# Kernel optimization log

Hardware: AMD Instinct MI355X
Metric: run time of the kernel (lower is better)

The kernel has to match this reference:

```python
import jax, jax.numpy as jnp
import numpy as np

NOTE_RES = 64  # global constant in the original repo; equals D of rep


def _down(x):
    # conv1d with kernel [0.5, 0.5], stride 2 over last axis (even length)
    return 0.5 * (x[..., ::2] + x[..., 1::2])


def setup_inputs() -> dict:
    key = jax.random.key(0)
    k1, k2, k3 = jax.random.split(key, 3)
    B, D, T = 32, NOTE_RES, 4096
    rep = jax.random.normal(k1, (B, D, T), dtype=jnp.float32)
    duration_mask = jax.random.uniform(k2, (B, D, T), dtype=jnp.float32)
    position_mask = jax.random.uniform(k3, (B, D, T), dtype=jnp.float32)
    return {
        "rep": rep,
        "duration_mask": duration_mask,
        "position_mask": position_mask,
        "low_duration": 1,
        "up_duration": 64,
    }


def reference(rep, duration_mask, position_mask, low_duration, up_duration):
    B, D, T = rep.shape  # D == NOTE_RES
    x = jnp.transpose(rep, (0, 2, 1))  # [B, T, NOTE_RES]; conv axis is last
    densed = _down(x)                  # [B, T, NOTE_RES//2]
    pot = NOTE_RES // 2
    res = jnp.zeros((B, T), dtype=rep.dtype)
    for i in range(0, NOTE_RES - low_duration):
        win_len = NOTE_RES - i - 1
        if win_len == pot:
            # descend one pyramid level
            x = densed
            densed = _down(x) if i < NOTE_RES - 2 else None
            d = x  # [B, T, win_len]
            pot //= 2
        else:
            pad_len = win_len - pot
            # mix fine-resolution prefix with coarse suffix -> length win_len
            d = jnp.concatenate([x[..., : 2 * pad_len], densed[..., pad_len:]], axis=-1)
        if win_len < up_duration:
            # sum_w d[b,t,w] * position_mask[b,w,t], gated by duration_mask[b,win_len-1,t]
            contrib = duration_mask[:, win_len - 1, :] * jnp.einsum(
                "btw,bwt->bt", d, position_mask[:, :win_len, :]
            )
            res = res + contrib
    return res[:, None, :]  # [B, 1, T]
```

## Files before the change

kernel.cpp:

```cpp
#include <hip/hip_runtime.h>


#define TT 4096

template <int K0>
__device__ __forceinline__ float roleK(const float* __restrict__ lrep,
                                       const float* __restrict__ lpm,
                                       const float* __restrict__ ldm, int lane,
                                       int low, int up) {
  constexpr int PADN = (K0 + 8 < 32) ? (K0 + 8) : 32;
  constexpr int PMN = (2 * K0 + 14 < 62 ? 2 * K0 + 14 : 62) - K0 + 1;
  float xa[8];
#pragma unroll
  for (int i = 0; i < 8; ++i)
    xa[i] = 0.5f * (lrep[(2 * (K0 + i)) * 64 + lane] +
                    lrep[(2 * (K0 + i) + 1) * 64 + lane]);
  float pmv[PMN];
#pragma unroll
  for (int r = 0; r < PMN; ++r) pmv[r] = lpm[(K0 + r) * 64 + lane];
  float res = 0.f;
#pragma unroll
  for (int pad = 0; pad < PADN; ++pad) {
    const int L = 32 + pad;
    const int kk0 = (pad > K0) ? pad : K0;
    float s = 0.f;
#pragma unroll
    for (int k = kk0; k < K0 + 8; ++k)
      s = fmaf(xa[k - K0], pmv[k + pad - K0], s);
    if (L >= low && L < up) res = fmaf(ldm[(31 + pad) * 64 + lane], s, res);
  }
  return res;
}

__device__ __forceinline__ float role3(const float* __restrict__ lrep,
                                       const float* __restrict__ lpm,
                                       const float* __restrict__ ldm, int lane,
                                       int low, int up) {
  float pmv[31];
#pragma unroll
  for (int r = 0; r < 31; ++r) pmv[r] = lpm[r * 64 + lane];
  float x1[32];
#pragma unroll
  for (int j = 0; j < 32; ++j)
    x1[j] = 0.5f * (lrep[(2 * j) * 64 + lane] + lrep[(2 * j + 1) * 64 + lane]);
  float res = 0.f;
#pragma unroll
  for (int pad = 0; pad < 8; ++pad) {
    const int L = 32 + pad;
    float s = 0.f;
#pragma unroll
    for (int k = pad; k < 8; ++k) s = fmaf(x1[k], pmv[k + pad], s);
    if (L >= low && L < up) res = fmaf(ldm[(31 + pad) * 64 + lane], s, res);
  }
  float x2[16], q1[16];
#pragma unroll
  for (int j = 0; j < 16; ++j) {
    const float a = x1[2 * j], bb = x1[2 * j + 1];
    x2[j] = 0.5f * (a + bb);
    q1[j] = a * pmv[2 * j] + bb * pmv[2 * j + 1];
  }
  float p = 0.f;
#pragma unroll
  for (int pad = 0; pad < 16; ++pad) {
    const int L = 16 + pad;
    float s = p;
#pragma unroll
    for (int k = pad; k < 16; ++k) s = fmaf(x2[k], pmv[k + pad], s);
    if (L >= low && L < up) res = fmaf(ldm[(15 + pad) * 64 + lane], s, res);
    p += q1[pad];
  }
  return res;
}

__device__ __forceinline__ float role4(const float* __restrict__ lrep,
                                       const float* __restrict__ lpm,
                                       const float* __restrict__ ldm, int lane,
                                       int low, int up) {
  float res = 0.f, p = 0.f;
#pragma unroll
  for (int pad = 1; pad < 32; ++pad) {
    const int j = pad - 1;
    p = fmaf(lrep[(2 * j) * 64 + lane], lpm[(2 * j) * 64 + lane],
             fmaf(lrep[(2 * j + 1) * 64 + lane], lpm[(2 * j + 1) * 64 + lane],
                  p));
    const int L = 32 + pad;
    if (L >= low && L < up) res = fmaf(ldm[(31 + pad) * 64 + lane], p, res);
  }
  return res;
}

template <int M>
__device__ __forceinline__ void level_step(const float* pmv,
                                           const float* __restrict__ ldm,
                                           int lane, int low, int up, float* xf,
                                           float* xc, float& res) {
  float q[M];
#pragma unroll
  for (int j = 0; j < M; ++j) {
    const float a = xf[2 * j], bb = xf[2 * j + 1];
    xc[j] = 0.5f * (a + bb);
    q[j] = a * pmv[2 * j] + bb * pmv[2 * j + 1];
  }
  float p = 0.f;
#pragma unroll
  for (int pad = 0; pad < M; ++pad) {
    const int L = M + pad;
    float s = p;
#pragma unroll
    for (int k = pad; k < M; ++k) s = fmaf(xc[k], pmv[k + pad], s);
    if (L >= low && L < up) res = fmaf(ldm[(M - 1 + pad) * 64 + lane], s, res);
    p += q[pad];
  }
}

__device__ __forceinline__ float role5(const float* __restrict__ lrep,
                                       const float* __restrict__ lpm,
                                       const float* __restrict__ ldm, int lane,
                                       int low, int up) {
  float pmv[15];
#pragma unroll
  for (int r = 0; r < 15; ++r) pmv[r] = lpm[r * 64 + lane];
  float x1[32];
#pragma unroll
  for (int j = 0; j < 32; ++j)
    x1[j] = 0.5f * (lrep[(2 * j) * 64 + lane] + lrep[(2 * j + 1) * 64 + lane]);
  float x2[16];
#pragma unroll
  for (int j = 0; j < 16; ++j) x2[j] = 0.5f * (x1[2 * j] + x1[2 * j + 1]);
  float res = 0.f;
  float x3[8], x4[4], x5[2], x6[1];
  level_step<8>(pmv, ldm, lane, low, up, x2, x3, res);
  level_step<4>(pmv, ldm, lane, low, up, x3, x4, res);
  level_step<2>(pmv, ldm, lane, low, up, x4, x5, res);
  level_step<1>(pmv, ldm, lane, low, up, x5, x6, res);
  return res;
}

__global__ __launch_bounds__(384, 3) void ContextGenerator_34875134444049_kernel(
    const float* __restrict__ rep, const float* __restrict__ dm,
    const float* __restrict__ pm, const int* __restrict__ lowp,
    const int* __restrict__ upp, float* __restrict__ out) {
  __shared__ float lds[192 * 64 + 6 * 64];
  const int tid = threadIdx.x;
  const int wid = tid >> 6;
  const int lane = tid & 63;
  const int b = blockIdx.x >> 6;
  const int t0 = (blockIdx.x & 63) << 6;
  const size_t base = (size_t)b * 64 * TT + (size_t)t0;

  float4 v[8];
#pragma unroll
  for (int g = 0; g < 8; ++g) {
    const int slot = tid + 384 * g;
    const int row = slot >> 4;
    const int c4 = (slot & 15) << 2;
    const float* tb = (row < 64) ? rep + base + (size_t)row * TT
                    : (row < 128) ? pm + base + (size_t)(row - 64) * TT
                                  : dm + base + (size_t)(row - 128) * TT;
    v[g] = *(const float4*)(tb + c4);
  }
#pragma unroll
  for (int g = 0; g < 8; ++g) {
    const int slot = tid + 384 * g;
    *(float4*)(&lds[slot << 2]) = v[g];
  }

  const int low = lowp[0];
  const int up = upp[0];

  __syncthreads();

  const float* lrep = lds;
  const float* lpm = lds + 64 * 64;
  const float* ldm = lds + 128 * 64;
  float* part = lds + 192 * 64;

  float res;
  if (wid == 0)
    res = roleK<24>(lrep, lpm, ldm, lane, low, up);
  else if (wid == 1)
    res = roleK<16>(lrep, lpm, ldm, lane, low, up);
  else if (wid == 2)
    res = roleK<8>(lrep, lpm, ldm, lane, low, up);
  else if (wid == 3)
    res = role3(lrep, lpm, ldm, lane, low, up);
  else if (wid == 4)
    res = role4(lrep, lpm, ldm, lane, low, up);
  else
    res = role5(lrep, lpm, ldm, lane, low, up);

  if (wid > 0) part[wid * 64 + lane] = res;
  __syncthreads();
  if (wid == 0)
    out[(size_t)b * TT + t0 + lane] = res + part[64 + lane] + part[128 + lane] +
                                      part[192 + lane] + part[256 + lane] +
                                      part[320 + lane];
}

extern "C" void kernel_launch(void* const* d_in, const int* in_sizes, int n_in,
                              void* d_out, int out_size, void* d_ws,
                              size_t ws_size, hipStream_t stream) {
  const float* rep = (const float*)d_in[0];
  const float* dm = (const float*)d_in[1];
  const float* pm = (const float*)d_in[2];
  const int* lowp = (const int*)d_in[3];
  const int* upp = (const int*)d_in[4];
  float* out = (float*)d_out;

  const int blocks = out_size / 64;
  ContextGenerator_34875134444049_kernel<<<blocks, 384, 0, stream>>>(
      rep, dm, pm, lowp, upp, out);
}
```

Before: 122.6 us.

## Make blocks persistent over four chunks and prefetch the next chunk during compute

Each block now handles four consecutive 64-column chunks instead of one. The global loads for chunk i+1 are issued into registers before chunk i's compute and written to LDS after the second barrier, so memory latency overlaps with the FMA work. This cuts the grid to a quarter of its former size, which lowers occupancy and wave-level parallelism in exchange for that software pipelining. It also keeps 8 float4 registers live across the compute roles, which may raise register pressure under the 384x3 launch bounds.

```diff
diff --git a/kernel.cpp b/kernel.cpp
--- a/kernel.cpp
+++ b/kernel.cpp
@@ -2,6 +2,7 @@
 
 
 #define TT 4096
+#define NCHUNK 4
 
 template <int K0>
 __device__ __forceinline__ float roleK(const float* __restrict__ lrep,
@@ -144,57 +145,90 @@
   const int tid = threadIdx.x;
   const int wid = tid >> 6;
   const int lane = tid & 63;
-  const int b = blockIdx.x >> 6;
-  const int t0 = (blockIdx.x & 63) << 6;
-  const size_t base = (size_t)b * 64 * TT + (size_t)t0;
-
-  float4 v[8];
-#pragma unroll
-  for (int g = 0; g < 8; ++g) {
-    const int slot = tid + 384 * g;
-    const int row = slot >> 4;
-    const int c4 = (slot & 15) << 2;
-    const float* tb = (row < 64) ? rep + base + (size_t)row * TT
-                    : (row < 128) ? pm + base + (size_t)(row - 64) * TT
-                                  : dm + base + (size_t)(row - 128) * TT;
-    v[g] = *(const float4*)(tb + c4);
-  }
-#pragma unroll
-  for (int g = 0; g < 8; ++g) {
-    const int slot = tid + 384 * g;
-    *(float4*)(&lds[slot << 2]) = v[g];
-  }
 
   const int low = lowp[0];
   const int up = upp[0];
 
-  __syncthreads();
+  const int c0 = blockIdx.x * NCHUNK;
+
+  float4 v[8];
+
+  {
+    const int c = c0;
+    const size_t base = (size_t)(c >> 6) * 64 * TT + (size_t)((c & 63) << 6);
+#pragma unroll
+    for (int g = 0; g < 8; ++g) {
+      const int slot = tid + 384 * g;
+      const int row = slot >> 4;
+      const int c4 = (slot & 15) << 2;
+      const float* tb = (row < 64) ? rep + base + (size_t)row * TT
+                      : (row < 128) ? pm + base + (size_t)(row - 64) * TT
+                                    : dm + base + (size_t)(row - 128) * TT;
+      v[g] = *(const float4*)(tb + c4);
+    }
+#pragma unroll
+    for (int g = 0; g < 8; ++g) {
+      const int slot = tid + 384 * g;
+      *(float4*)(&lds[slot << 2]) = v[g];
+    }
+  }
 
   const float* lrep = lds;
   const float* lpm = lds + 64 * 64;
   const float* ldm = lds + 128 * 64;
   float* part = lds + 192 * 64;
 
-  float res;
-  if (wid == 0)
-    res = roleK<24>(lrep, lpm, ldm, lane, low, up);
-  else if (wid == 1)
-    res = roleK<16>(lrep, lpm, ldm, lane, low, up);
-  else if (wid == 2)
-    res = roleK<8>(lrep, lpm, ldm, lane, low, up);
-  else if (wid == 3)
-    res = role3(lrep, lpm, ldm, lane, low, up);
-  else if (wid == 4)
-    res = role4(lrep, lpm, ldm, lane, low, up);
-  else
-    res = role5(lrep, lpm, ldm, lane, low, up);
-
-  if (wid > 0) part[wid * 64 + lane] = res;
-  __syncthreads();
-  if (wid == 0)
-    out[(size_t)b * TT + t0 + lane] = res + part[64 + lane] + part[128 + lane] +
-                                      part[192 + lane] + part[256 + lane] +
-                                      part[320 + lane];
+#pragma unroll 1
+  for (int i = 0; i < NCHUNK; ++i) {
+    __syncthreads();
+
+    if (i + 1 < NCHUNK) {
+      const int c = c0 + i + 1;
+      const size_t base = (size_t)(c >> 6) * 64 * TT + (size_t)((c & 63) << 6);
+#pragma unroll
+      for (int g = 0; g < 8; ++g) {
+        const int slot = tid + 384 * g;
+        const int row = slot >> 4;
+        const int c4 = (slot & 15) << 2;
+        const float* tb = (row < 64) ? rep + base + (size_t)row * TT
+                        : (row < 128) ? pm + base + (size_t)(row - 64) * TT
+                                      : dm + base + (size_t)(row - 128) * TT;
+        v[g] = *(const float4*)(tb + c4);
+      }
+    }
+
+    float res;
+    if (wid == 0)
+      res = roleK<24>(lrep, lpm, ldm, lane, low, up);
+    else if (wid == 1)
+      res = roleK<16>(lrep, lpm, ldm, lane, low, up);
+    else if (wid == 2)
+      res = roleK<8>(lrep, lpm, ldm, lane, low, up);
+    else if (wid == 3)
+      res = role3(lrep, lpm, ldm, lane, low, up);
+    else if (wid == 4)
+      res = role4(lrep, lpm, ldm, lane, low, up);
+    else
+      res = role5(lrep, lpm, ldm, lane, low, up);
+
+    if (wid > 0) part[wid * 64 + lane] = res;
+    __syncthreads();
+
+    if (wid == 0) {
+      const int c = c0 + i;
+      out[(size_t)(c >> 6) * TT + (size_t)((c & 63) << 6) + lane] =
+          res + part[64 + lane] + part[128 + lane] + part[192 + lane] +
+          part[256 + lane] + part[320 + lane];
+    }
+
+    if (i + 1 < NCHUNK) {
+#pragma unroll
+      for (int g = 0; g < 8; ++g) {
+        const int slot = tid + 384 * g;
+        *(float4*)(&lds[slot << 2]) = v[g];
+      }
+    }
+  }
 }
 
 extern "C" void kernel_launch(void* const* d_in, const int* in_sizes, int n_in,
@@ -207,7 +241,7 @@
   const int* upp = (const int*)d_in[4];
   float* out = (float*)d_out;
 
-  const int blocks = out_size / 64;
+  const int blocks = out_size / (64 * NCHUNK);
   ContextGenerator_34875134444049_kernel<<<blocks, 384, 0, stream>>>(
       rep, dm, pm, lowp, upp, out);
 }
```

Result: slower. 164.1 us (+33.8%).
